# Kernel optimization log

Measured on AMD Instinct MI355X. Metric: run time of the kernel, lower is better.

The kernel has to match this reference:

```python
import jax, jax.numpy as jnp
import numpy as np

NEG_SLOPE = 0.2


def setup_inputs() -> dict:
    key = jax.random.key(0)
    ks = jax.random.split(key, 5)
    B, N, QD, KD, H = 32, 16384, 128, 128, 128
    query = jax.random.normal(ks[0], (B, QD), dtype=jnp.float32)
    key_t = jax.random.normal(ks[1], (B, N, KD), dtype=jnp.float32)
    # nn.Linear weights: out = x @ W.T ; scale roughly like torch default init
    Wq = jax.random.normal(ks[2], (H, QD), dtype=jnp.float32) / np.sqrt(QD)
    Wk = jax.random.normal(ks[3], (H, KD), dtype=jnp.float32) / np.sqrt(KD)
    Wa = jax.random.normal(ks[4], (H,), dtype=jnp.float32) / np.sqrt(H)
    return {"query": query, "key": key_t, "Wq": Wq, "Wk": Wk, "Wa": Wa}


def reference(query, key, Wq, Wk, Wa):
    # query: [B, QD], key: [B, N, KD]
    h_query = jnp.einsum('bq,hq->bh', query, Wq)          # [B, H]
    h_key = jnp.einsum('bnk,hk->bnh', key, Wk)            # [B, N, H]
    h = h_query[:, None, :] + h_key                       # broadcast add
    e = jax.nn.leaky_relu(h, negative_slope=NEG_SLOPE)
    e = jnp.einsum('bnh,h->bn', e, Wa)                    # rank-1 attention
    e = jax.nn.softmax(e, axis=-1)                        # [B, N]
    scored = jnp.einsum('bnh,bn->bh', h_key, e)           # weighted sum over nodes
    h_prime = jax.nn.elu(scored)
    return h_prime, e
```

## Files before the change

### kernel.cpp

```cpp
#include <hip/hip_runtime.h>
#include <math.h>

#define B_ 32
#define N_ 16384
#define D_ 128
#define NEG_SLOPE 0.2f
#define CHUNKS 16
#define TILE 64
#define ITERS 16

typedef __attribute__((ext_vector_type(8))) short short8;
typedef __attribute__((ext_vector_type(4))) float f32x4;

__device__ __forceinline__ unsigned short f2bf(float x) {
    union { float f; unsigned int u; } v; v.f = x;
    unsigned int r = v.u + 0x7FFFu + ((v.u >> 16) & 1u);
    return (unsigned short)(r >> 16);
}

__global__ void hq_kernel(const float* __restrict__ query,
                          const float* __restrict__ Wq,
                          float* __restrict__ hq) {
    int b = blockIdx.x, h = threadIdx.x;
    const float4* q4 = (const float4*)(query + (size_t)b * D_);
    const float4* w4 = (const float4*)(Wq + (size_t)h * D_);
    float s = 0.f;
#pragma unroll
    for (int k = 0; k < D_ / 4; ++k) {
        float4 q = q4[k], w = w4[k];
        s += q.x * w.x + q.y * w.y + q.z * w.z + q.w * w.w;
    }
    hq[b * D_ + h] = s;
}

__global__ __launch_bounds__(256, 2) void
main_kernel(const float* __restrict__ key, const float* __restrict__ Wk,
            const float* __restrict__ Wa, const float* __restrict__ hq,
            float* __restrict__ logits, float* __restrict__ part) {
    __shared__ float kbuf[2][TILE * D_];
    __shared__ float comb_acc[4][D_];
    __shared__ float comb_m[4], comb_l[4];

    const int b = blockIdx.y, chunk = blockIdx.x;
    const int tid = threadIdx.x;
    const int w = tid >> 6;
    const int lane = tid & 63;
    const int ln = lane & 15;
    const int g = lane >> 4;
    const int n0 = chunk * (N_ / CHUNKS);

    short8 bfrag[8][4];
#pragma unroll
    for (int cf = 0; cf < 8; ++cf) {
        const float* wp = Wk + (size_t)(cf * 16 + ln) * D_;
#pragma unroll
        for (int kk = 0; kk < 4; ++kk) {
            const float4* p = (const float4*)(wp + kk * 32 + g * 8);
            float4 x = p[0], y = p[1];
            short8 f;
            f[0] = f2bf(x.x); f[1] = f2bf(x.y); f[2] = f2bf(x.z); f[3] = f2bf(x.w);
            f[4] = f2bf(y.x); f[5] = f2bf(y.y); f[6] = f2bf(y.z); f[7] = f2bf(y.w);
            bfrag[cf][kk] = f;
        }
    }
    float hq_r[8], wa_r[8];
#pragma unroll
    for (int cf = 0; cf < 8; ++cf) {
        hq_r[cf] = hq[b * D_ + cf * 16 + ln];
        wa_r[cf] = Wa[cf * 16 + ln];
    }

    float m_w = -1e30f, l_w = 0.f;
    float accl[8];
#pragma unroll
    for (int cf = 0; cf < 8; ++cf) accl[cf] = 0.f;

    const char* kbase = (const char*)(key + ((size_t)b * N_ + n0) * D_);

    auto stage = [&](int it) {
        const char* gt = kbase + (size_t)it * (TILE * D_ * 4);
        char* lb = (char*)&kbuf[it & 1][0];
#pragma unroll
        for (int k = 0; k < 8; ++k) {
            unsigned Loff = (unsigned)(w * 8192 + k * 1024 + lane * 16);
            unsigned sw = ((Loff >> 9) & 7u) << 4;
            __builtin_amdgcn_global_load_lds(
                (const __attribute__((address_space(1))) unsigned int*)(uintptr_t)(gt + (Loff ^ sw)),
                (__attribute__((address_space(3))) unsigned int*)(uintptr_t)(lb + w * 8192 + k * 1024),
                16, 0, 0);
        }
    };

    stage(0);
    for (int it = 0; it < ITERS; ++it) {
        if (it + 1 < ITERS) {
            stage(it + 1);
            asm volatile("s_waitcnt vmcnt(8)" ::: "memory");
        } else {
            asm volatile("s_waitcnt vmcnt(0)" ::: "memory");
        }
        const char* lb = (const char*)&kbuf[it & 1][0];
        const int r = w * 16 + ln;
        const unsigned sw = (unsigned)(r & 7) << 4;

        f32x4 acc[8] = {};
#pragma unroll
        for (int kk = 0; kk < 4; ++kk) {
            unsigned off0 = (unsigned)(r * 512 + kk * 128 + g * 32);
            float4 x = *(const float4*)(lb + (off0 ^ sw));
            float4 y = *(const float4*)(lb + ((off0 + 16) ^ sw));
            short8 a;
            a[0] = f2bf(x.x); a[1] = f2bf(x.y); a[2] = f2bf(x.z); a[3] = f2bf(x.w);
            a[4] = f2bf(y.x); a[5] = f2bf(y.y); a[6] = f2bf(y.z); a[7] = f2bf(y.w);
#pragma unroll
            for (int cf = 0; cf < 8; ++cf)
                acc[cf] = __builtin_amdgcn_mfma_f32_16x16x32_bf16(a, bfrag[cf][kk], acc[cf], 0, 0, 0);
        }

        float lg[4];
#pragma unroll
        for (int j = 0; j < 4; ++j) {
            float s = 0.f;
#pragma unroll
            for (int cf = 0; cf < 8; ++cf) {
                float v = hq_r[cf] + acc[cf][j];
                v = (v > 0.f) ? v : (NEG_SLOPE * v);
                s = fmaf(v, wa_r[cf], s);
            }
            s += __shfl_xor(s, 1);
            s += __shfl_xor(s, 2);
            s += __shfl_xor(s, 4);
            s += __shfl_xor(s, 8);
            lg[j] = s;
        }
        int nbase = n0 + it * TILE + w * 16;
        if (ln == 0)
            *(float4*)&logits[(size_t)b * N_ + nbase + g * 4] =
                make_float4(lg[0], lg[1], lg[2], lg[3]);

        float mt = fmaxf(fmaxf(lg[0], lg[1]), fmaxf(lg[2], lg[3]));
        mt = fmaxf(mt, __shfl_xor(mt, 16));
        mt = fmaxf(mt, __shfl_xor(mt, 32));
        float m_new = fmaxf(m_w, mt);
        float corr = __expf(m_w - m_new);
        l_w *= corr;
#pragma unroll
        for (int cf = 0; cf < 8; ++cf) accl[cf] *= corr;
#pragma unroll
        for (int j = 0; j < 4; ++j) {
            float p = __expf(lg[j] - m_new);
            l_w += (ln == 0) ? p : 0.f;
#pragma unroll
            for (int cf = 0; cf < 8; ++cf)
                accl[cf] = fmaf(p, acc[cf][j], accl[cf]);
        }
        m_w = m_new;
    }

#pragma unroll
    for (int cf = 0; cf < 8; ++cf) {
        accl[cf] += __shfl_xor(accl[cf], 16);
        accl[cf] += __shfl_xor(accl[cf], 32);
    }
    l_w += __shfl_xor(l_w, 1);
    l_w += __shfl_xor(l_w, 2);
    l_w += __shfl_xor(l_w, 4);
    l_w += __shfl_xor(l_w, 8);
    l_w += __shfl_xor(l_w, 16);
    l_w += __shfl_xor(l_w, 32);
    if (lane < 16) {
#pragma unroll
        for (int cf = 0; cf < 8; ++cf)
            comb_acc[w][cf * 16 + ln] = accl[cf];
    }
    if (lane == 0) { comb_m[w] = m_w; comb_l[w] = l_w; }
    __syncthreads();
    if (tid < D_) {
        float mb = fmaxf(fmaxf(comb_m[0], comb_m[1]), fmaxf(comb_m[2], comb_m[3]));
        float lb = 0.f, ab = 0.f;
#pragma unroll
        for (int ww = 0; ww < 4; ++ww) {
            float cw = __expf(comb_m[ww] - mb);
            lb = fmaf(comb_l[ww], cw, lb);
            ab = fmaf(comb_acc[ww][tid], cw, ab);
        }
        float* pp = part + ((size_t)b * CHUNKS + chunk) * 132;
        pp[2 + tid] = ab;
        if (tid == 0) pp[0] = mb;
        if (tid == 1) pp[1] = lb;
    }
}

__global__ void finish_kernel(const float* __restrict__ part,
                              float* __restrict__ out_hp,
                              float* __restrict__ mblb) {
    int b = blockIdx.x, h = threadIdx.x;
    float mb = -1e30f;
    for (int c = 0; c < CHUNKS; ++c)
        mb = fmaxf(mb, part[((size_t)b * CHUNKS + c) * 132]);
    float lb = 0.f, ac = 0.f;
    for (int c = 0; c < CHUNKS; ++c) {
        const float* pp = part + ((size_t)b * CHUNKS + c) * 132;
        float cw = __expf(pp[0] - mb);
        lb = fmaf(pp[1], cw, lb);
        ac = fmaf(pp[2 + h], cw, ac);
    }
    float scored = ac / lb;
    out_hp[b * D_ + h] = (scored > 0.f) ? scored : expm1f(scored);
    if (h == 0) { mblb[b * 2] = mb; mblb[b * 2 + 1] = lb; }
}

__global__ void e_kernel(const float* __restrict__ logits,
                         const float* __restrict__ mblb,
                         float* __restrict__ out_e) {
    int idx = blockIdx.x * blockDim.x + threadIdx.x;
    int n4 = idx * 4;
    int b = n4 >> 14;
    float mb = mblb[b * 2];
    float inv = 1.f / mblb[b * 2 + 1];
    float4 lg = *(const float4*)&logits[(size_t)n4];
    float4 e;
    e.x = __expf(lg.x - mb) * inv;
    e.y = __expf(lg.y - mb) * inv;
    e.z = __expf(lg.z - mb) * inv;
    e.w = __expf(lg.w - mb) * inv;
    *(float4*)&out_e[(size_t)n4] = e;
}

extern "C" void kernel_launch(void* const* d_in, const int* in_sizes, int n_in,
                              void* d_out, int out_size, void* d_ws, size_t ws_size,
                              hipStream_t stream) {
    const float* query = (const float*)d_in[0];
    const float* key   = (const float*)d_in[1];
    const float* Wq    = (const float*)d_in[2];
    const float* Wk    = (const float*)d_in[3];
    const float* Wa    = (const float*)d_in[4];
    float* out = (float*)d_out;

    float* ws     = (float*)d_ws;
    float* hq     = ws;
    float* logits = ws + 4096;
    float* part   = logits + (size_t)B_ * N_;
    float* mblb   = part + (size_t)B_ * CHUNKS * 132;

    hq_kernel<<<dim3(B_), dim3(D_), 0, stream>>>(query, Wq, hq);
    main_kernel<<<dim3(CHUNKS, B_), dim3(256), 0, stream>>>(key, Wk, Wa, hq, logits, part);
    finish_kernel<<<dim3(B_), dim3(D_), 0, stream>>>(part, out, mblb);
    e_kernel<<<dim3((B_ * N_ / 4) / 256), dim3(256), 0, stream>>>(logits, mblb, out + B_ * D_);
}
```

Baseline: 80.74 us.

## Fuse hq and finish kernels, split tiles into halves with deeper LDS pipeline

Computes the query projection inside the main kernel instead of a separate launch, and merges the finish and e-normalization kernels into one, cutting the launch count from four to two. The key staging is split into half-tiles (64 columns) with a four-slot LDS ring and three stages in flight, so loads overlap more with MFMA. Scalar bf16 conversion is replaced with packed float2-to-bfloat162 intrinsics. Risks include redundant hq computation per block, each finish_e block recomputing the chunk-combine reduction, and hand-tuned vmcnt waits that must match the exact number of loads in flight.

```diff
diff --git a/kernel.cpp b/kernel.cpp
--- a/kernel.cpp
+++ b/kernel.cpp
@@ -1,4 +1,5 @@
 #include <hip/hip_runtime.h>
+#include <hip/hip_bf16.h>
 #include <math.h>
 
 #define B_ 32
@@ -6,38 +7,47 @@
 #define D_ 128
 #define NEG_SLOPE 0.2f
 #define CHUNKS 16
-#define TILE 64
 #define ITERS 16
 
 typedef __attribute__((ext_vector_type(8))) short short8;
 typedef __attribute__((ext_vector_type(4))) float f32x4;
 
-__device__ __forceinline__ unsigned short f2bf(float x) {
-    union { float f; unsigned int u; } v; v.f = x;
-    unsigned int r = v.u + 0x7FFFu + ((v.u >> 16) & 1u);
-    return (unsigned short)(r >> 16);
-}
-
-__global__ void hq_kernel(const float* __restrict__ query,
-                          const float* __restrict__ Wq,
-                          float* __restrict__ hq) {
-    int b = blockIdx.x, h = threadIdx.x;
-    const float4* q4 = (const float4*)(query + (size_t)b * D_);
-    const float4* w4 = (const float4*)(Wq + (size_t)h * D_);
-    float s = 0.f;
-#pragma unroll
-    for (int k = 0; k < D_ / 4; ++k) {
-        float4 q = q4[k], w = w4[k];
-        s += q.x * w.x + q.y * w.y + q.z * w.z + q.w * w.w;
-    }
-    hq[b * D_ + h] = s;
-}
+__device__ __forceinline__ short8 cvt8(float4 x, float4 y) {
+    union { unsigned u[4]; short8 s; } r;
+    union { __hip_bfloat162 b; unsigned u; } t;
+    t.b = __float22bfloat162_rn(make_float2(x.x, x.y)); r.u[0] = t.u;
+    t.b = __float22bfloat162_rn(make_float2(x.z, x.w)); r.u[1] = t.u;
+    t.b = __float22bfloat162_rn(make_float2(y.x, y.y)); r.u[2] = t.u;
+    t.b = __float22bfloat162_rn(make_float2(y.z, y.w)); r.u[3] = t.u;
+    return r.s;
+}
+
+template<int HALF>
+__device__ __forceinline__ void compute_half(const char* lbuf, int ln, int g, int w,
+                                             const short8 (&bfrag)[8][4], f32x4 (&acc)[8]) {
+    const int r = w * 16 + ln;
+    const unsigned swr = (unsigned)(ln & 7) << 4;
+#pragma unroll
+    for (int kk2 = 0; kk2 < 2; ++kk2) {
+        unsigned off0 = (unsigned)(r * 256 + kk2 * 128 + g * 32);
+        float4 x = *(const float4*)(lbuf + (off0 ^ swr));
+        float4 y = *(const float4*)(lbuf + ((off0 + 16) ^ swr));
+        short8 a = cvt8(x, y);
+#pragma unroll
+        for (int cf = 0; cf < 8; ++cf)
+            acc[cf] = __builtin_amdgcn_mfma_f32_16x16x32_bf16(
+                a, bfrag[cf][HALF * 2 + kk2], acc[cf], 0, 0, 0);
+    }
+}
+
+#define WAITV(N) asm volatile("s_waitcnt vmcnt(" #N ")" ::: "memory")
 
 __global__ __launch_bounds__(256, 2) void
-main_kernel(const float* __restrict__ key, const float* __restrict__ Wk,
-            const float* __restrict__ Wa, const float* __restrict__ hq,
+main_kernel(const float* __restrict__ query, const float* __restrict__ key,
+            const float* __restrict__ Wq, const float* __restrict__ Wk,
+            const float* __restrict__ Wa,
             float* __restrict__ logits, float* __restrict__ part) {
-    __shared__ float kbuf[2][TILE * D_];
+    __shared__ float kbuf[4][64 * 64];
     __shared__ float comb_acc[4][D_];
     __shared__ float comb_m[4], comb_l[4];
 
@@ -56,18 +66,27 @@
 #pragma unroll
         for (int kk = 0; kk < 4; ++kk) {
             const float4* p = (const float4*)(wp + kk * 32 + g * 8);
-            float4 x = p[0], y = p[1];
-            short8 f;
-            f[0] = f2bf(x.x); f[1] = f2bf(x.y); f[2] = f2bf(x.z); f[3] = f2bf(x.w);
-            f[4] = f2bf(y.x); f[5] = f2bf(y.y); f[6] = f2bf(y.z); f[7] = f2bf(y.w);
-            bfrag[cf][kk] = f;
+            bfrag[cf][kk] = cvt8(p[0], p[1]);
         }
     }
     float hq_r[8], wa_r[8];
-#pragma unroll
-    for (int cf = 0; cf < 8; ++cf) {
-        hq_r[cf] = hq[b * D_ + cf * 16 + ln];
-        wa_r[cf] = Wa[cf * 16 + ln];
+    {
+        const float4* qv = (const float4*)(query + (size_t)b * D_);
+#pragma unroll
+        for (int cf = 0; cf < 8; ++cf) {
+            const float4* wv = (const float4*)(Wq + (size_t)(cf * 16 + ln) * D_ + g * 32);
+            float s = 0.f;
+#pragma unroll
+            for (int u = 0; u < 8; ++u) {
+                float4 wq = wv[u], qq = qv[g * 8 + u];
+                s = fmaf(wq.x, qq.x, s); s = fmaf(wq.y, qq.y, s);
+                s = fmaf(wq.z, qq.z, s); s = fmaf(wq.w, qq.w, s);
+            }
+            s += __shfl_xor(s, 16);
+            s += __shfl_xor(s, 32);
+            hq_r[cf] = s;
+            wa_r[cf] = Wa[cf * 16 + ln];
+        }
     }
 
     float m_w = -1e30f, l_w = 0.f;
@@ -76,45 +95,46 @@
     for (int cf = 0; cf < 8; ++cf) accl[cf] = 0.f;
 
     const char* kbase = (const char*)(key + ((size_t)b * N_ + n0) * D_);
-
-    auto stage = [&](int it) {
-        const char* gt = kbase + (size_t)it * (TILE * D_ * 4);
-        char* lb = (char*)&kbuf[it & 1][0];
-#pragma unroll
-        for (int k = 0; k < 8; ++k) {
-            unsigned Loff = (unsigned)(w * 8192 + k * 1024 + lane * 16);
-            unsigned sw = ((Loff >> 9) & 7u) << 4;
+    char* lds0 = (char*)&kbuf[0][0];
+
+    auto stage = [&](int s) {
+        const int itt = s >> 1, half = s & 1;
+        const char* gt = kbase + (size_t)itt * (64 * 512) + half * 256;
+        char* lb = lds0 + (s & 3) * 16384 + w * 4096;
+        const int rr = lane >> 4;
+        const unsigned cb = (unsigned)(lane & 15) * 16;
+#pragma unroll
+        for (int k = 0; k < 4; ++k) {
+            int rowk = k * 4 + rr;
+            unsigned src = (unsigned)((w * 16 + rowk) * 512) +
+                           (cb ^ (((unsigned)(rowk & 7)) << 4));
             __builtin_amdgcn_global_load_lds(
-                (const __attribute__((address_space(1))) unsigned int*)(uintptr_t)(gt + (Loff ^ sw)),
-                (__attribute__((address_space(3))) unsigned int*)(uintptr_t)(lb + w * 8192 + k * 1024),
+                (const __attribute__((address_space(1))) unsigned int*)(uintptr_t)(gt + src),
+                (__attribute__((address_space(3))) unsigned int*)(uintptr_t)(lb + k * 1024),
                 16, 0, 0);
         }
     };
 
-    stage(0);
+    stage(0); stage(1); stage(2);
+
     for (int it = 0; it < ITERS; ++it) {
-        if (it + 1 < ITERS) {
-            stage(it + 1);
-            asm volatile("s_waitcnt vmcnt(8)" ::: "memory");
-        } else {
-            asm volatile("s_waitcnt vmcnt(0)" ::: "memory");
-        }
-        const char* lb = (const char*)&kbuf[it & 1][0];
-        const int r = w * 16 + ln;
-        const unsigned sw = (unsigned)(r & 7) << 4;
-
         f32x4 acc[8] = {};
-#pragma unroll
-        for (int kk = 0; kk < 4; ++kk) {
-            unsigned off0 = (unsigned)(r * 512 + kk * 128 + g * 32);
-            float4 x = *(const float4*)(lb + (off0 ^ sw));
-            float4 y = *(const float4*)(lb + ((off0 + 16) ^ sw));
-            short8 a;
-            a[0] = f2bf(x.x); a[1] = f2bf(x.y); a[2] = f2bf(x.z); a[3] = f2bf(x.w);
-            a[4] = f2bf(y.x); a[5] = f2bf(y.y); a[6] = f2bf(y.z); a[7] = f2bf(y.w);
-#pragma unroll
-            for (int cf = 0; cf < 8; ++cf)
-                acc[cf] = __builtin_amdgcn_mfma_f32_16x16x32_bf16(a, bfrag[cf][kk], acc[cf], 0, 0, 0);
+        {
+            int s = 2 * it;
+            if (s + 3 < 32) stage(s + 3);
+            if (it == 0)      WAITV(12);
+            else if (it < 15) WAITV(13);
+            else              WAITV(6);
+            compute_half<0>(lds0 + (s & 3) * 16384, ln, g, w, bfrag, acc);
+        }
+        {
+            int s = 2 * it + 1;
+            if (s + 3 < 32) stage(s + 3);
+            if (it == 0)       WAITV(12);
+            else if (it < 14)  WAITV(13);
+            else if (it == 14) WAITV(9);
+            else               WAITV(1);
+            compute_half<1>(lds0 + (s & 3) * 16384, ln, g, w, bfrag, acc);
         }
 
         float lg[4];
@@ -133,7 +153,7 @@
             s += __shfl_xor(s, 8);
             lg[j] = s;
         }
-        int nbase = n0 + it * TILE + w * 16;
+        int nbase = n0 + it * 64 + w * 16;
         if (ln == 0)
             *(float4*)&logits[(size_t)b * N_ + nbase + g * 4] =
                 make_float4(lg[0], lg[1], lg[2], lg[3]);
@@ -191,40 +211,39 @@
     }
 }
 
-__global__ void finish_kernel(const float* __restrict__ part,
-                              float* __restrict__ out_hp,
-                              float* __restrict__ mblb) {
-    int b = blockIdx.x, h = threadIdx.x;
+__global__ __launch_bounds__(256) void
+finish_e_kernel(const float* __restrict__ part, const float* __restrict__ logits,
+                float* __restrict__ out) {
+    const int b = blockIdx.y, s = blockIdx.x, t = threadIdx.x;
     float mb = -1e30f;
+#pragma unroll
     for (int c = 0; c < CHUNKS; ++c)
         mb = fmaxf(mb, part[((size_t)b * CHUNKS + c) * 132]);
-    float lb = 0.f, ac = 0.f;
+    float lb = 0.f;
+#pragma unroll
     for (int c = 0; c < CHUNKS; ++c) {
         const float* pp = part + ((size_t)b * CHUNKS + c) * 132;
-        float cw = __expf(pp[0] - mb);
-        lb = fmaf(pp[1], cw, lb);
-        ac = fmaf(pp[2 + h], cw, ac);
-    }
-    float scored = ac / lb;
-    out_hp[b * D_ + h] = (scored > 0.f) ? scored : expm1f(scored);
-    if (h == 0) { mblb[b * 2] = mb; mblb[b * 2 + 1] = lb; }
-}
-
-__global__ void e_kernel(const float* __restrict__ logits,
-                         const float* __restrict__ mblb,
-                         float* __restrict__ out_e) {
-    int idx = blockIdx.x * blockDim.x + threadIdx.x;
-    int n4 = idx * 4;
-    int b = n4 >> 14;
-    float mb = mblb[b * 2];
-    float inv = 1.f / mblb[b * 2 + 1];
-    float4 lg = *(const float4*)&logits[(size_t)n4];
+        lb = fmaf(pp[1], __expf(pp[0] - mb), lb);
+    }
+    if (s == 0 && t < D_) {
+        float ac = 0.f;
+#pragma unroll
+        for (int c = 0; c < CHUNKS; ++c) {
+            const float* pp = part + ((size_t)b * CHUNKS + c) * 132;
+            ac = fmaf(pp[2 + t], __expf(pp[0] - mb), ac);
+        }
+        float sc = ac / lb;
+        out[b * D_ + t] = (sc > 0.f) ? sc : expm1f(sc);
+    }
+    float inv = 1.f / lb;
+    int n4 = s * 1024 + t * 4;
+    float4 lg = *(const float4*)&logits[(size_t)b * N_ + n4];
     float4 e;
     e.x = __expf(lg.x - mb) * inv;
     e.y = __expf(lg.y - mb) * inv;
     e.z = __expf(lg.z - mb) * inv;
     e.w = __expf(lg.w - mb) * inv;
-    *(float4*)&out_e[(size_t)n4] = e;
+    *(float4*)&out[(size_t)B_ * D_ + (size_t)b * N_ + n4] = e;
 }
 
 extern "C" void kernel_launch(void* const* d_in, const int* in_sizes, int n_in,
@@ -238,13 +257,9 @@
     float* out = (float*)d_out;
 
     float* ws     = (float*)d_ws;
-    float* hq     = ws;
-    float* logits = ws + 4096;
+    float* logits = ws;
     float* part   = logits + (size_t)B_ * N_;
-    float* mblb   = part + (size_t)B_ * CHUNKS * 132;
-
-    hq_kernel<<<dim3(B_), dim3(D_), 0, stream>>>(query, Wq, hq);
-    main_kernel<<<dim3(CHUNKS, B_), dim3(256), 0, stream>>>(key, Wk, Wa, hq, logits, part);
-    finish_kernel<<<dim3(B_), dim3(D_), 0, stream>>>(part, out, mblb);
-    e_kernel<<<dim3((B_ * N_ / 4) / 256), dim3(256), 0, stream>>>(logits, mblb, out + B_ * D_);
-}
+
+    main_kernel<<<dim3(CHUNKS, B_), dim3(256), 0, stream>>>(query, key, Wq, Wk, Wa, logits, part);
+    finish_e_kernel<<<dim3(16, B_), dim3(256), 0, stream>>>(part, logits, out);
+}
```

Result: no change. 79.62 us (-1.4%).
